# Optimization experiments

Hardware: AMD Instinct MI355X
Metric: run time of the kernel (lower is better)

## Reference

```python
import jax, jax.numpy as jnp
import numpy as np

EPS_BN = 1e-5
EPS_NORM = 1e-12
NUM_HEADS = 8


def _bn_relu(x):
    # BatchNorm2d in training mode with fresh params (gamma=1, beta=0), then ReLU.
    m = x.mean((0, 2, 3), keepdims=True)
    v = x.var((0, 2, 3), keepdims=True)  # biased variance, as PyTorch uses for normalization
    return jax.nn.relu((x - m) * jax.lax.rsqrt(v + EPS_BN))


def _conv3(x, w, groups=1):
    # 3x3 conv, stride 1, padding 1 (NCHW / OIHW)
    return jax.lax.conv_general_dilated(
        x, w, (1, 1), ((1, 1), (1, 1)),
        dimension_numbers=('NCHW', 'OIHW', 'NCHW'),
        feature_group_count=groups)


def _encoder(x, w1, w2, w3):
    # Conv1x1 -> BN -> ReLU -> Conv k2 s2 -> BN -> ReLU -> Conv1x1 -> BN -> ReLU
    x = _bn_relu(jnp.einsum('bihw,oi->bohw', x, w1))
    b, c, h, w = x.shape
    # k=2,s=2 conv as a reshape + einsum (non-overlapping 2x2 patches)
    x = _bn_relu(jnp.einsum('bchpwq,ocpq->bohw', x.reshape(b, c, h // 2, 2, w // 2, 2), w2))
    return _bn_relu(jnp.einsum('bihw,oi->bohw', x, w3))


def _decoder(x, w1, w2, w3):
    # ConvT1x1 -> BN -> ReLU -> ConvT k2 s2 -> BN -> ReLU -> ConvT1x1 -> BN -> ReLU
    x = _bn_relu(jnp.einsum('bihw,io->bohw', x, w1))
    # ConvTranspose k=2,s=2: each input pixel expands to a 2x2 block
    y = jnp.einsum('bihw,iopq->bohpwq', x, w2)
    b, o, h, p, w, q = y.shape
    x = _bn_relu(y.reshape(b, o, h * p, w * q))
    return _bn_relu(jnp.einsum('bihw,io->bohw', x, w3))


def _l2norm(x):
    # F.normalize(dim=-1) with eps=1e-12
    return x / jnp.maximum(jnp.linalg.norm(x, axis=-1, keepdims=True), EPS_NORM)


def setup_inputs() -> dict:
    key = jax.random.key(0)
    ks = jax.random.split(key, 13)
    B, C, H, W = 8, 256, 64, 64
    d = C // 4  # attention dim after self.divide

    def rn(k, shape, s=0.1):
        return jax.random.normal(k, shape, jnp.float32) * s

    return {
        'x': jax.random.normal(ks[0], (B, C, H, W), jnp.float32),
        'y': jax.random.normal(ks[1], (B, C, H, W), jnp.float32),
        'temperature': jnp.ones((NUM_HEADS, 1, 1), jnp.float32),
        'enc_w1': rn(ks[2], (d // 2, C)),
        'enc_w2': rn(ks[3], (d // 2, d // 2, 2, 2)),
        'enc_w3': rn(ks[4], (d, d // 2)),
        'kv_w': rn(ks[5], (2 * d, d)),
        'kv_dw_w': rn(ks[6], (2 * d, 1, 3, 3)),
        'q_w': rn(ks[7], (d, d)),
        'q_dw_w': rn(ks[8], (d, d, 3, 3)),
        'proj_w': rn(ks[9], (d, d)),
        'dec_w1': rn(ks[10], (d, 2 * d)),
        'dec_w2': rn(ks[11], (2 * d, 2 * d, 2, 2)),
        'dec_w3': rn(ks[12], (2 * d, 4 * d)),
    }


def reference(x, y, temperature, enc_w1, enc_w2, enc_w3, kv_w, kv_dw_w,
              q_w, q_dw_w, proj_w, dec_w1, dec_w2, dec_w3):
    # Shared freshly-built encoder applied to both x and y (same weights,
    # BN batch stats computed per call).
    x = _encoder(x, enc_w1, enc_w2, enc_w3)
    y = _encoder(y, enc_w1, enc_w2, enc_w3)
    b, c, h, w = x.shape  # c = 64, h = w = 32

    kv = _conv3(jnp.einsum('bihw,oi->bohw', x, kv_w), kv_dw_w, groups=2 * c)
    k, v = jnp.split(kv, 2, axis=1)
    q = _conv3(jnp.einsum('bihw,oi->bohw', y, q_w), q_dw_w)  # regular 3x3 conv

    ch = c // NUM_HEADS
    heads = lambda t: t.reshape(b, NUM_HEADS, ch, h * w)  # b head c (h w)
    q, k, v = heads(q), heads(k), heads(v)
    q = _l2norm(q)
    k = _l2norm(k)
    temp = temperature[None]  # [1, head, 1, 1]

    # Spatial attention: [b, head, hw, hw]
    attn_s = jax.nn.softmax(jnp.einsum('bhcn,bhcm->bhnm', q, k) * temp, axis=-1)
    out_s = jnp.einsum('bhcn,bhnm->bhcm', v, attn_s).reshape(b, c, h, w)
    out_s = jnp.einsum('bihw,oi->bohw', out_s, proj_w)

    # Channel attention: [b, head, c, c]
    attn_c = jax.nn.softmax(jnp.einsum('bhcn,bhdn->bhcd', q, k) * temp, axis=-1)
    out_c = jnp.einsum('bhcd,bhdn->bhcn', attn_c, v).reshape(b, c, h, w)
    out_c = jnp.einsum('bihw,oi->bohw', out_c, proj_w)

    return _decoder(out_s + out_c, dec_w1, dec_w2, dec_w3)
```

## Files before the change

### kernel.cpp

```cpp
#include <hip/hip_runtime.h>
#include <hip/hip_bf16.h>

#define EPS_BN 1e-5f

__global__ __launch_bounds__(256) void conv1x1_enc1_kernel(
    const float* __restrict__ in0, const float* __restrict__ in1,
    const float* __restrict__ w, float* __restrict__ out,
    float* __restrict__ stOut)
{
  __shared__ float il[32*128];
  __shared__ float wt[32*32];
  int tid  = threadIdx.x;
  int tile = blockIdx.x;
  int z    = blockIdx.y;
  int t    = z >> 3;
  const float* in  = t ? in1 : in0;
  const float* inb = in + ((size_t)(z&7))*256*4096 + tile*128;
  int cg = tid & 31;
  int og = tid >> 5;

  float acc[4][4];
#pragma unroll
  for(int j=0;j<4;j++){ acc[j][0]=acc[j][1]=acc[j][2]=acc[j][3]=0.f; }

  for(int k0=0; k0<256; k0+=32){
    __syncthreads();
#pragma unroll
    for(int u=0;u<4;u++){
      int fid = tid + u*256;
      int ch = fid >> 5, c4 = fid & 31;
      ((float4*)il)[fid] = *(const float4*)(inb + (size_t)(k0+ch)*4096 + c4*4);
    }
#pragma unroll
    for(int u=0;u<4;u++){
      int idx = tid + u*256;
      int o = idx >> 5, ch = idx & 31;
      wt[ch*32 + o] = w[(size_t)o*256 + k0 + ch];
    }
    __syncthreads();
#pragma unroll 8
    for(int ch=0; ch<32; ch++){
      float4 v  = ((float4*)il)[ch*32 + cg];
      float4 wv = ((float4*)wt)[ch*8 + og];
      acc[0][0]=fmaf(wv.x,v.x,acc[0][0]); acc[0][1]=fmaf(wv.x,v.y,acc[0][1]);
      acc[0][2]=fmaf(wv.x,v.z,acc[0][2]); acc[0][3]=fmaf(wv.x,v.w,acc[0][3]);
      acc[1][0]=fmaf(wv.y,v.x,acc[1][0]); acc[1][1]=fmaf(wv.y,v.y,acc[1][1]);
      acc[1][2]=fmaf(wv.y,v.z,acc[1][2]); acc[1][3]=fmaf(wv.y,v.w,acc[1][3]);
      acc[2][0]=fmaf(wv.z,v.x,acc[2][0]); acc[2][1]=fmaf(wv.z,v.y,acc[2][1]);
      acc[2][2]=fmaf(wv.z,v.z,acc[2][2]); acc[2][3]=fmaf(wv.z,v.w,acc[2][3]);
      acc[3][0]=fmaf(wv.w,v.x,acc[3][0]); acc[3][1]=fmaf(wv.w,v.y,acc[3][1]);
      acc[3][2]=fmaf(wv.w,v.z,acc[3][2]); acc[3][3]=fmaf(wv.w,v.w,acc[3][3]);
    }
  }

  float* ob = out + ((size_t)z*32 + og*4)*4096 + tile*128 + cg*4;
#pragma unroll
  for(int j=0;j<4;j++){
    float4 vv = {acc[j][0],acc[j][1],acc[j][2],acc[j][3]};
    *(float4*)(ob + (size_t)j*4096) = vv;
  }
#pragma unroll
  for(int j=0;j<4;j++){
    float s  = acc[j][0]+acc[j][1]+acc[j][2]+acc[j][3];
    float s2 = acc[j][0]*acc[j][0]+acc[j][1]*acc[j][1]
             + acc[j][2]*acc[j][2]+acc[j][3]*acc[j][3];
    for(int off=16; off>0; off>>=1){
      s  += __shfl_down(s,  off, 64);
      s2 += __shfl_down(s2, off, 64);
    }
    if((tid & 31)==0){
      atomicAdd(&stOut[((size_t)t*32 + og*4 + j)*2],   s);
      atomicAdd(&stOut[((size_t)t*32 + og*4 + j)*2+1], s2);
    }
  }
}

template<int OT, bool HASBN, bool HASSTATS>
__global__ __launch_bounds__(256) void conv1x1_kernel(
    const float* __restrict__ in0, const float* __restrict__ in1,
    const float* __restrict__ w, float* __restrict__ out,
    const float* __restrict__ stIn, float* __restrict__ stOut,
    int I, int O, int P, int wio, int zsplit, float invN)
{
  __shared__ float wl[2048];
  __shared__ float bnm[256], bnr[256];
  int tid = threadIdx.x;
  int o0 = blockIdx.y*OT;
  int z  = blockIdx.z;
  int t  = (z >= zsplit) ? 1 : 0;
  int b  = t ? (z - zsplit) : z;
  const float* in = t ? in1 : in0;

  for(int idx=tid; idx<I*OT; idx+=256){
    int i = idx/OT, j = idx - i*OT;
    wl[idx] = wio ? w[(size_t)i*O + o0 + j] : w[(size_t)(o0+j)*I + i];
  }
  if(HASBN){
    for(int i=tid; i<I; i+=256){
      float s  = stIn[((size_t)t*I + i)*2];
      float s2 = stIn[((size_t)t*I + i)*2+1];
      float m  = s*invN;
      bnm[i] = m;
      bnr[i] = rsqrtf(s2*invN - m*m + EPS_BN);
    }
  }
  __syncthreads();

  int p4 = blockIdx.x*256 + tid;
  const float4* inb = (const float4*)(in + (size_t)b*I*P) + p4;
  int P4 = P >> 2;

  float acc[OT][4];
#pragma unroll
  for(int j=0;j<OT;j++){ acc[j][0]=acc[j][1]=acc[j][2]=acc[j][3]=0.f; }

  float4 vb[8];
  for(int i0=0;i0<I;i0+=8){
#pragma unroll
    for(int u=0;u<8;u++) vb[u] = inb[(size_t)(i0+u)*P4];
#pragma unroll
    for(int u=0;u<8;u++){
      float4 v = vb[u];
      if(HASBN){
        float m = bnm[i0+u], r = bnr[i0+u];
        v.x = fmaxf((v.x-m)*r, 0.f); v.y = fmaxf((v.y-m)*r, 0.f);
        v.z = fmaxf((v.z-m)*r, 0.f); v.w = fmaxf((v.w-m)*r, 0.f);
      }
      const float* wr = &wl[(i0+u)*OT];
#pragma unroll
      for(int j=0;j<OT;j++){
        float wv = wr[j];
        acc[j][0] = fmaf(wv, v.x, acc[j][0]);
        acc[j][1] = fmaf(wv, v.y, acc[j][1]);
        acc[j][2] = fmaf(wv, v.z, acc[j][2]);
        acc[j][3] = fmaf(wv, v.w, acc[j][3]);
      }
    }
  }

  float4* ob = (float4*)(out + ((size_t)z*O + o0)*P) + p4;
#pragma unroll
  for(int j=0;j<OT;j++){
    float4 vv = {acc[j][0], acc[j][1], acc[j][2], acc[j][3]};
    ob[(size_t)j*P4] = vv;
  }

  if(HASSTATS){
#pragma unroll
    for(int j=0;j<OT;j++){
      float s  = acc[j][0]+acc[j][1]+acc[j][2]+acc[j][3];
      float s2 = acc[j][0]*acc[j][0]+acc[j][1]*acc[j][1]
               + acc[j][2]*acc[j][2]+acc[j][3]*acc[j][3];
      for(int off=32; off>0; off>>=1){
        s  += __shfl_down(s,  off, 64);
        s2 += __shfl_down(s2, off, 64);
      }
      if((tid & 63)==0){
        atomicAdd(&stOut[((size_t)t*O + o0 + j)*2],   s);
        atomicAdd(&stOut[((size_t)t*O + o0 + j)*2+1], s2);
      }
    }
  }
}

__global__ __launch_bounds__(256) void conv2x2s2_bn_kernel(
    const float* __restrict__ in, const float* __restrict__ w,
    float* __restrict__ out, const float* __restrict__ stIn,
    float* __restrict__ stOut, float invN)
{
  __shared__ float wl[512];
  __shared__ float bnm[32], bnr[32];
  int tid = threadIdx.x;
  int o0 = blockIdx.x*4;
  int z  = blockIdx.y;
  int t  = (z >= 8) ? 1 : 0;

  for(int idx=tid; idx<512; idx+=256){
    int pq = idx & 3, r = idx >> 2;
    int i = r >> 2, j = r & 3;
    wl[idx] = w[(((size_t)(o0+j)*32 + i)*4) + pq];
  }
  if(tid < 32){
    float s  = stIn[((size_t)t*32 + tid)*2];
    float s2 = stIn[((size_t)t*32 + tid)*2+1];
    float m  = s*invN;
    bnm[tid] = m;
    bnr[tid] = rsqrtf(s2*invN - m*m + EPS_BN);
  }
  __syncthreads();

  int h  = tid >> 3;
  int wg = tid & 7;
  int cb = wg*8;

  float acc[4][4];
#pragma unroll
  for(int j=0;j<4;j++) for(int k=0;k<4;k++) acc[j][k]=0.f;

  float4 pre[8];
  for(int i0=0;i0<32;i0+=4){
#pragma unroll
    for(int u=0;u<4;u++){
      pre[2*u]   = *(const float4*)(in + (((size_t)z*32+i0+u)*64 + 2*h)*64 + cb);
      pre[2*u+1] = *(const float4*)(in + (((size_t)z*32+i0+u)*64 + 2*h)*64 + cb + 4);
    }
#pragma unroll
    for(int u=0;u<4;u++){
      int i = i0+u;
      const float4* r1p = (const float4*)(in + (((size_t)z*32+i)*64 + 2*h+1)*64 + cb);
      float4 a0 = pre[2*u], a1 = pre[2*u+1];
      float4 b0 = r1p[0], b1 = r1p[1];
      float m = bnm[i], r = bnr[i];
      float t0[8] = {a0.x,a0.y,a0.z,a0.w,a1.x,a1.y,a1.z,a1.w};
      float t1[8] = {b0.x,b0.y,b0.z,b0.w,b1.x,b1.y,b1.z,b1.w};
#pragma unroll
      for(int e=0;e<8;e++){
        t0[e] = fmaxf((t0[e]-m)*r, 0.f);
        t1[e] = fmaxf((t1[e]-m)*r, 0.f);
      }
#pragma unroll
      for(int j=0;j<4;j++){
        const float* wj = &wl[(i*4+j)*4];
#pragma unroll
        for(int k=0;k<4;k++){
          acc[j][k] = fmaf(wj[0], t0[2*k],   acc[j][k]);
          acc[j][k] = fmaf(wj[1], t0[2*k+1], acc[j][k]);
          acc[j][k] = fmaf(wj[2], t1[2*k],   acc[j][k]);
          acc[j][k] = fmaf(wj[3], t1[2*k+1], acc[j][k]);
        }
      }
    }
  }

#pragma unroll
  for(int j=0;j<4;j++){
    float4 vv = {acc[j][0],acc[j][1],acc[j][2],acc[j][3]};
    *(float4*)(out + ((size_t)z*32 + o0+j)*1024 + h*32 + wg*4) = vv;
  }
#pragma unroll
  for(int j=0;j<4;j++){
    float s  = acc[j][0]+acc[j][1]+acc[j][2]+acc[j][3];
    float s2 = acc[j][0]*acc[j][0]+acc[j][1]*acc[j][1]
             + acc[j][2]*acc[j][2]+acc[j][3]*acc[j][3];
    for(int off=32; off>0; off>>=1){
      s  += __shfl_down(s,  off, 64);
      s2 += __shfl_down(s2, off, 64);
    }
    if((tid & 63)==0){
      atomicAdd(&stOut[((size_t)t*32 + o0 + j)*2],   s);
      atomicAdd(&stOut[((size_t)t*32 + o0 + j)*2+1], s2);
    }
  }
}

__global__ __launch_bounds__(256) void upsample2x2_bn_kernel(
    const float* __restrict__ in, const float* __restrict__ w,
    float* __restrict__ out, const float* __restrict__ stIn,
    float* __restrict__ stOut, float invN)
{
  __shared__ float wl[1024];
  __shared__ float bnm[128], bnr[128];
  int tid = threadIdx.x;
  int o0 = blockIdx.x*2;
  int b  = blockIdx.y;

  for(int idx=tid; idx<1024; idx+=256){
    int pq = idx & 3, r = idx >> 2;
    int i = r >> 1, j = r & 1;
    wl[idx] = w[((size_t)i*128 + o0+j)*4 + pq];
  }
  if(tid < 128){
    float s  = stIn[(size_t)tid*2];
    float s2 = stIn[(size_t)tid*2+1];
    float m  = s*invN;
    bnm[tid] = m;
    bnr[tid] = rsqrtf(s2*invN - m*m + EPS_BN);
  }
  __syncthreads();

  int h  = tid >> 3;
  int wg = tid & 7;
  int w0 = wg*4;

  float acc[2][16];
#pragma unroll
  for(int j=0;j<2;j++) for(int e=0;e<16;e++) acc[j][e]=0.f;

  float4 vb4[8];
  for(int i0=0;i0<128;i0+=8){
#pragma unroll
    for(int u=0;u<8;u++)
      vb4[u] = *(const float4*)(in + (((size_t)b*128+i0+u)*1024) + h*32 + w0);
#pragma unroll
    for(int u=0;u<8;u++){
      int i = i0+u;
      float4 v = vb4[u];
      float m = bnm[i], r = bnr[i];
      float vk[4] = {fmaxf((v.x-m)*r,0.f), fmaxf((v.y-m)*r,0.f),
                     fmaxf((v.z-m)*r,0.f), fmaxf((v.w-m)*r,0.f)};
#pragma unroll
      for(int j=0;j<2;j++){
        const float* wj = &wl[(i*2+j)*4];
#pragma unroll
        for(int pq=0;pq<4;pq++){
#pragma unroll
          for(int k=0;k<4;k++)
            acc[j][pq*4+k] = fmaf(wj[pq], vk[k], acc[j][pq*4+k]);
        }
      }
    }
  }

#pragma unroll
  for(int j=0;j<2;j++){
    float* ob = out + ((size_t)b*128 + o0+j)*4096;
#pragma unroll
    for(int p=0;p<2;p++){
      float4 A = {acc[j][(p*2+0)*4+0], acc[j][(p*2+1)*4+0],
                  acc[j][(p*2+0)*4+1], acc[j][(p*2+1)*4+1]};
      float4 B = {acc[j][(p*2+0)*4+2], acc[j][(p*2+1)*4+2],
                  acc[j][(p*2+0)*4+3], acc[j][(p*2+1)*4+3]};
      *(float4*)(ob + (2*h+p)*64 + 2*w0)     = A;
      *(float4*)(ob + (2*h+p)*64 + 2*w0 + 4) = B;
    }
  }

#pragma unroll
  for(int j=0;j<2;j++){
    float s=0.f, s2=0.f;
#pragma unroll
    for(int e=0;e<16;e++){ s += acc[j][e]; s2 += acc[j][e]*acc[j][e]; }
    for(int off=32; off>0; off>>=1){
      s  += __shfl_down(s,  off, 64);
      s2 += __shfl_down(s2, off, 64);
    }
    if((tid & 63)==0){
      atomicAdd(&stOut[((size_t)(o0+j))*2],   s);
      atomicAdd(&stOut[((size_t)(o0+j))*2+1], s2);
    }
  }
}

__global__ __launch_bounds__(256) void bn_final_kernel(
    float* __restrict__ x, const float* __restrict__ st, float invN)
{
  int idx4 = blockIdx.x*256 + threadIdx.x;
  int c = (idx4 >> 10) & 255;
  float s  = st[(size_t)c*2];
  float s2 = st[(size_t)c*2+1];
  float m  = s*invN;
  float r  = rsqrtf(s2*invN - m*m + EPS_BN);
  float4 v = ((float4*)x)[idx4];
  v.x = fmaxf((v.x-m)*r, 0.f); v.y = fmaxf((v.y-m)*r, 0.f);
  v.z = fmaxf((v.z-m)*r, 0.f); v.w = fmaxf((v.w-m)*r, 0.f);
  ((float4*)x)[idx4] = v;
}

__global__ __launch_bounds__(256) void dwconv3x3_kernel(
    const float* __restrict__ in, const float* __restrict__ w,
    float* __restrict__ out, int C, int H, int Wd)
{
  int idx = blockIdx.x*256 + threadIdx.x;
  int c = blockIdx.y, b = blockIdx.z;
  if(idx >= H*Wd) return;
  int h = idx / Wd, x = idx - h*Wd;
  const float* inp = in + ((size_t)b*C + c)*H*Wd;
  float acc = 0.f;
#pragma unroll
  for(int p=0;p<3;p++){
    int hh = h + p - 1;
    if((unsigned)hh >= (unsigned)H) continue;
#pragma unroll
    for(int q=0;q<3;q++){
      int wv = x + q - 1;
      if((unsigned)wv >= (unsigned)Wd) continue;
      acc += w[c*9 + p*3 + q] * inp[hh*Wd + wv];
    }
  }
  out[((size_t)b*C + c)*H*Wd + idx] = acc;
}

__global__ __launch_bounds__(256) void conv3x3_kernel(
    const float* __restrict__ in, const float* __restrict__ w,
    float* __restrict__ out, int IC, int H, int Wd)
{
  int o = blockIdx.y, b = blockIdx.z;
  __shared__ float wl[576];
  for(int t=threadIdx.x; t<IC*9; t+=256) wl[t] = w[(size_t)o*IC*9 + t];
  __syncthreads();
  int idx = blockIdx.x*256 + threadIdx.x;
  if(idx >= H*Wd) return;
  int h = idx / Wd, x = idx - h*Wd;
  const float* inb = in + (size_t)b*IC*H*Wd;
  float acc = 0.f;
  for(int i=0;i<IC;i++){
    const float* inp = inb + (size_t)i*H*Wd;
    const float* wp  = wl + i*9;
#pragma unroll
    for(int p=0;p<3;p++){
      int hh = h + p - 1;
      if((unsigned)hh >= (unsigned)H) continue;
      const float* row = inp + hh*Wd;
#pragma unroll
      for(int q=0;q<3;q++){
        int wv = x + q - 1;
        if((unsigned)wv >= (unsigned)Wd) continue;
        acc = fmaf(wp[p*3+q], row[wv], acc);
      }
    }
  }
  out[((size_t)b*gridDim.y + o)*H*Wd + idx] = acc;
}

__global__ __launch_bounds__(256) void l2norm_kernel(
    float* __restrict__ q, float* __restrict__ kv)
{
  int r = blockIdx.x;
  float* p;
  if(r < 512){ int b=r>>6, c=r&63; p = q + ((size_t)b*64+c)*1024; }
  else { int rr=r-512; int b=rr>>6, c=rr&63; p = kv + ((size_t)b*128+c)*1024; }
  int tid = threadIdx.x;
  float4 v = ((float4*)p)[tid];
  float s = v.x*v.x + v.y*v.y + v.z*v.z + v.w*v.w;
  __shared__ float ls[256];
  ls[tid]=s; __syncthreads();
  for(int st=128; st>0; st>>=1){ if(tid<st) ls[tid]+=ls[tid+st]; __syncthreads(); }
  float scale = 1.f / fmaxf(sqrtf(ls[0]), 1e-12f);
  v.x*=scale; v.y*=scale; v.z*=scale; v.w*=scale;
  ((float4*)p)[tid] = v;
}

__global__ __launch_bounds__(256) void attn_pass1(
    const float* __restrict__ q, const float* __restrict__ kv,
    const float* __restrict__ temp, float* __restrict__ den_out)
{
  int bx = blockIdx.x, hh = blockIdx.y, b = blockIdx.z;
  int nchunk = bx >> 1, mh = bx & 1;
  int tid = threadIdx.x;
  __shared__ __align__(16) float kl[512*12];
  const float* kb = kv + ((size_t)b*128 + hh*8)*1024 + mh*512;
  for(int t=tid;t<4096;t+=256){ int c=t>>9, m=t&511; kl[m*12+c]=kb[(size_t)c*1024+m]; }
  __syncthreads();
  int n = nchunk*256 + tid;
  const float* qp = q + ((size_t)b*64 + hh*8)*1024 + n;
  float th = temp[hh];
  float mxb = fabsf(th);
  float qr[8];
#pragma unroll
  for(int c=0;c<8;c++) qr[c]=qp[(size_t)c*1024]*th;
  const float4* kl4 = (const float4*)kl;
  float den = 0.f, den2 = 0.f;
  for(int m=0;m<512;m+=2){
    float4 a  = kl4[m*3],     a2 = kl4[m*3+1];
    float4 bt = kl4[(m+1)*3], b2 = kl4[(m+1)*3+1];
    float s0 = qr[0]*a.x+qr[1]*a.y+qr[2]*a.z+qr[3]*a.w
             + qr[4]*a2.x+qr[5]*a2.y+qr[6]*a2.z+qr[7]*a2.w;
    float s1 = qr[0]*bt.x+qr[1]*bt.y+qr[2]*bt.z+qr[3]*bt.w
             + qr[4]*b2.x+qr[5]*b2.y+qr[6]*b2.z+qr[7]*b2.w;
    den  += __expf(s0 - mxb);
    den2 += __expf(s1 - mxb);
  }
  atomicAdd(&den_out[((size_t)(b*8+hh))*1024+n], den+den2);
}

__global__ __launch_bounds__(256) void attn_pass2(
    const float* __restrict__ q, const float* __restrict__ kv,
    const float* __restrict__ temp, const float* __restrict__ den,
    float* __restrict__ out)
{
  int bx = blockIdx.x, hh = blockIdx.y, b = blockIdx.z;
  int mchunk = bx >> 1, nh = bx & 1;
  int tid = threadIdx.x;
  __shared__ __align__(16) float ql[512*12];
  __shared__ __align__(16) float vl[512*12];
  __shared__ float idl[512];
  int bh = b*8+hh;
  int n0 = nh*512;
  const float* qb = q  + ((size_t)b*64 + hh*8)*1024 + n0;
  const float* vb = kv + ((size_t)b*128 + 64 + hh*8)*1024 + n0;
  for(int t=tid;t<4096;t+=256){
    int c=t>>9, n=t&511;
    ql[n*12+c] = qb[(size_t)c*1024+n];
    vl[n*12+c] = vb[(size_t)c*1024+n];
  }
  for(int u=tid;u<512;u+=256) idl[u] = 1.f/den[(size_t)bh*1024 + n0 + u];
  __syncthreads();
  int m = mchunk*256 + tid;
  const float* kb = kv + ((size_t)b*128 + hh*8)*1024 + m;
  float th = temp[hh];
  float mxb = fabsf(th);
  float kr[8];
#pragma unroll
  for(int c=0;c<8;c++) kr[c]=kb[(size_t)c*1024]*th;
  float acc[8] = {0,0,0,0,0,0,0,0};
  const float4* ql4 = (const float4*)ql;
  const float4* vl4 = (const float4*)vl;
  for(int n=0;n<512;n+=2){
    float4 qa = ql4[n*3],     qa2 = ql4[n*3+1];
    float4 qb4= ql4[(n+1)*3], qb2 = ql4[(n+1)*3+1];
    float s0 = kr[0]*qa.x+kr[1]*qa.y+kr[2]*qa.z+kr[3]*qa.w
             + kr[4]*qa2.x+kr[5]*qa2.y+kr[6]*qa2.z+kr[7]*qa2.w;
    float s1 = kr[0]*qb4.x+kr[1]*qb4.y+kr[2]*qb4.z+kr[3]*qb4.w
             + kr[4]*qb2.x+kr[5]*qb2.y+kr[6]*qb2.z+kr[7]*qb2.w;
    float p0 = __expf(s0 - mxb) * idl[n];
    float p1 = __expf(s1 - mxb) * idl[n+1];
    float4 va = vl4[n*3],     va2 = vl4[n*3+1];
    float4 vb4f= vl4[(n+1)*3], vb2 = vl4[(n+1)*3+1];
    acc[0]+=p0*va.x + p1*vb4f.x; acc[1]+=p0*va.y + p1*vb4f.y;
    acc[2]+=p0*va.z + p1*vb4f.z; acc[3]+=p0*va.w + p1*vb4f.w;
    acc[4]+=p0*va2.x + p1*vb2.x; acc[5]+=p0*va2.y + p1*vb2.y;
    acc[6]+=p0*va2.z + p1*vb2.z; acc[7]+=p0*va2.w + p1*vb2.w;
  }
  float* ob = out + ((size_t)b*64 + hh*8)*1024 + m;
#pragma unroll
  for(int c=0;c<8;c++) atomicAdd(&ob[(size_t)c*1024], acc[c]);
}

__global__ __launch_bounds__(256) void attn_channel(
    const float* __restrict__ q, const float* __restrict__ kv,
    const float* __restrict__ temp, float* out)
{
  int hh = blockIdx.x, b = blockIdx.y;
  __shared__ float kl[8192];
  const float* qb = q  + ((size_t)b*64 + hh*8)*1024;
  const float* kb = kv + ((size_t)b*128 + hh*8)*1024;
  const float* vb = kv + ((size_t)b*128 + 64 + hh*8)*1024;
  int tid = threadIdx.x;
  for(int t=tid;t<8192;t+=256) kl[t]=kb[t];
  __syncthreads();
  __shared__ float part[256];
  __shared__ float a[64];
  {
    int pair = tid >> 2, seg = tid & 3;
    int c = pair >> 3, d = pair & 7;
    const float* qrow = qb + (size_t)c*1024 + seg*256;
    const float* krow = kl + d*1024 + seg*256;
    float s = 0.f;
#pragma unroll 4
    for(int n=0;n<256;n++) s += qrow[n]*krow[n];
    part[tid] = s;
  }
  __syncthreads();
  if(tid < 64){
    float g = part[tid*4]+part[tid*4+1]+part[tid*4+2]+part[tid*4+3];
    part[tid] = g * temp[hh];
  }
  __syncthreads();
  if(tid < 8){
    float mx = -3.4e38f;
    for(int d=0;d<8;d++) mx = fmaxf(mx, part[tid*8+d]);
    float den = 0.f;
    float e[8];
    for(int d=0;d<8;d++){ e[d] = __expf(part[tid*8+d]-mx); den+=e[d]; }
    float inv = 1.f/den;
    for(int d=0;d<8;d++) a[tid*8+d] = e[d]*inv;
  }
  __syncthreads();
  float* ob = out + ((size_t)b*64 + hh*8)*1024;
  for(int n=tid;n<1024;n+=256){
    float vv[8];
#pragma unroll
    for(int d=0;d<8;d++) vv[d] = vb[(size_t)d*1024+n];
#pragma unroll
    for(int c=0;c<8;c++){
      float s = 0.f;
#pragma unroll
      for(int d=0;d<8;d++) s += a[c*8+d]*vv[d];
      ob[(size_t)c*1024+n] += s;
    }
  }
}

extern "C" void kernel_launch(void* const* d_in, const int* in_sizes, int n_in,
                              void* d_out, int out_size, void* d_ws, size_t ws_size,
                              hipStream_t stream)
{
  (void)in_sizes; (void)n_in; (void)out_size; (void)ws_size;
  const float* x      = (const float*)d_in[0];
  const float* y      = (const float*)d_in[1];
  const float* temp   = (const float*)d_in[2];
  const float* enc_w1 = (const float*)d_in[3];
  const float* enc_w2 = (const float*)d_in[4];
  const float* enc_w3 = (const float*)d_in[5];
  const float* kv_w   = (const float*)d_in[6];
  const float* kv_dw_w= (const float*)d_in[7];
  const float* q_w    = (const float*)d_in[8];
  const float* q_dw_w = (const float*)d_in[9];
  const float* proj_w = (const float*)d_in[10];
  const float* dec_w1 = (const float*)d_in[11];
  const float* dec_w2 = (const float*)d_in[12];
  const float* dec_w3 = (const float*)d_in[13];
  float* out = (float*)d_out;

  float* W   = (float*)d_ws;
  float* ST  = W;
  float* ST0 = ST;
  float* ST1 = ST + 128;
  float* ST2 = ST + 256;
  float* ST3 = ST + 512;
  float* ST4 = ST + 768;
  float* ST5 = ST + 1024;
  float* A    = W + 2048;
  float* E1   = A;
  float* KV1  = A;
  float* QPre = A + 1048576;
  float* ATTN = A;
  float* PROJ = A + 524288;
  float* D1   = A + 1048576;
  float* E2   = W + 2099200;
  float* E3   = W + 2623488;
  float* KV   = W + 3672064;
  float* Q    = W + 4720640;
  float* DEN  = W + 5244928;
  float* D2   = W + 2099200;

  const float inv32k = 1.f/32768.f, inv8k = 1.f/8192.f;

  hipMemsetAsync(ST, 0, 2048*sizeof(float), stream);
  hipMemsetAsync(DEN, 0, 65536*sizeof(float), stream);

  conv1x1_enc1_kernel<<<dim3(32,16),256,0,stream>>>(x, y, enc_w1, E1, ST0);
  conv2x2s2_bn_kernel<<<dim3(8,16),256,0,stream>>>(E1, enc_w2, E2, ST0, ST1, inv32k);
  conv1x1_kernel<2,true,true><<<dim3(1,32,16),256,0,stream>>>(
      E2, E2 + (size_t)8*32*1024, enc_w3, E3, ST1, ST2, 32, 64, 1024, 0, 8, inv8k);

  conv1x1_kernel<2,true,false><<<dim3(1,64,8),256,0,stream>>>(
      E3, E3, kv_w, KV1, ST2, nullptr, 64, 128, 1024, 0, 999, inv8k);
  dwconv3x3_kernel<<<dim3(4,128,8),256,0,stream>>>(KV1, kv_dw_w, KV, 128, 32, 32);
  conv1x1_kernel<2,true,false><<<dim3(1,32,8),256,0,stream>>>(
      E3 + (size_t)8*64*1024, E3, q_w, QPre, ST2 + 128, nullptr, 64, 64, 1024, 0, 999, inv8k);
  conv3x3_kernel<<<dim3(4,64,8),256,0,stream>>>(QPre, q_dw_w, Q, 64, 32, 32);

  hipMemsetAsync(ATTN, 0, 524288*sizeof(float), stream);

  l2norm_kernel<<<1024,256,0,stream>>>(Q, KV);

  attn_pass1<<<dim3(8,8,8),256,0,stream>>>(Q, KV, temp, DEN);
  attn_pass2<<<dim3(8,8,8),256,0,stream>>>(Q, KV, temp, DEN, ATTN);
  attn_channel<<<dim3(8,8),256,0,stream>>>(Q, KV, temp, ATTN);

  conv1x1_kernel<2,false,false><<<dim3(1,32,8),256,0,stream>>>(
      ATTN, ATTN, proj_w, PROJ, nullptr, nullptr, 64, 64, 1024, 0, 999, 0.f);

  conv1x1_kernel<2,false,true><<<dim3(1,64,8),256,0,stream>>>(
      PROJ, PROJ, dec_w1, D1, nullptr, ST3, 64, 128, 1024, 1, 999, 0.f);
  upsample2x2_bn_kernel<<<dim3(64,8),256,0,stream>>>(D1, dec_w2, D2, ST3, ST4, inv8k);
  conv1x1_kernel<8,true,true><<<dim3(4,32,8),256,0,stream>>>(
      D2, D2, dec_w3, out, ST4, ST5, 128, 256, 4096, 1, 999, inv32k);
  bn_final_kernel<<<8192,256,0,stream>>>(out, ST5, inv32k);
}
```

Measured before the change: 637.5 us.

## Raise grid parallelism across encoder, small 1x1 convs and spatial attention

Result: faster. 620.8 us (-2.6%).

```diff
diff --git a/kernel.cpp b/kernel.cpp
--- a/kernel.cpp
+++ b/kernel.cpp
@@ -8,69 +8,85 @@
     const float* __restrict__ w, float* __restrict__ out,
     float* __restrict__ stOut)
 {
-  __shared__ float il[32*128];
-  __shared__ float wt[32*32];
+  __shared__ float il[2][32*64];
+  __shared__ float wt[2][32*34];
   int tid  = threadIdx.x;
   int tile = blockIdx.x;
   int z    = blockIdx.y;
   int t    = z >> 3;
   const float* in  = t ? in1 : in0;
-  const float* inb = in + ((size_t)(z&7))*256*4096 + tile*128;
-  int cg = tid & 31;
-  int og = tid >> 5;
-
-  float acc[4][4];
-#pragma unroll
-  for(int j=0;j<4;j++){ acc[j][0]=acc[j][1]=acc[j][2]=acc[j][3]=0.f; }
-
-  for(int k0=0; k0<256; k0+=32){
-    __syncthreads();
-#pragma unroll
-    for(int u=0;u<4;u++){
-      int fid = tid + u*256;
-      int ch = fid >> 5, c4 = fid & 31;
-      ((float4*)il)[fid] = *(const float4*)(inb + (size_t)(k0+ch)*4096 + c4*4);
-    }
-#pragma unroll
-    for(int u=0;u<4;u++){
-      int idx = tid + u*256;
-      int o = idx >> 5, ch = idx & 31;
-      wt[ch*32 + o] = w[(size_t)o*256 + k0 + ch];
-    }
-    __syncthreads();
+  const float* inb = in + ((size_t)(z&7))*256*4096 + tile*64;
+  int cg = tid & 15;
+  int og = tid >> 4;
+
+  float4 vr[2]; float wr[4];
+  int chA = tid >> 4;
+  int chB = 16 + chA;
+  int wo  = tid >> 5;
+  int wch = tid & 31;
+
+  vr[0] = *(const float4*)(inb + (size_t)chA*4096 + cg*4);
+  vr[1] = *(const float4*)(inb + (size_t)chB*4096 + cg*4);
+#pragma unroll
+  for(int u=0;u<4;u++) wr[u] = w[(size_t)(wo+u*8)*256 + wch];
+  ((float4*)il[0])[tid]     = vr[0];
+  ((float4*)il[0])[tid+256] = vr[1];
+#pragma unroll
+  for(int u=0;u<4;u++) wt[0][wch*34 + wo + u*8] = wr[u];
+  __syncthreads();
+
+  float acc[2][4];
+#pragma unroll
+  for(int j=0;j<2;j++){ acc[j][0]=acc[j][1]=acc[j][2]=acc[j][3]=0.f; }
+
+  for(int c=0;c<8;c++){
+    int cur = c & 1;
+    if(c < 7){
+      int k0 = (c+1)*32;
+      vr[0] = *(const float4*)(inb + (size_t)(k0+chA)*4096 + cg*4);
+      vr[1] = *(const float4*)(inb + (size_t)(k0+chB)*4096 + cg*4);
+#pragma unroll
+      for(int u=0;u<4;u++) wr[u] = w[(size_t)(wo+u*8)*256 + k0 + wch];
+    }
+    const float4* ilc = (const float4*)il[cur];
+    const float*  wtc = wt[cur];
 #pragma unroll 8
     for(int ch=0; ch<32; ch++){
-      float4 v  = ((float4*)il)[ch*32 + cg];
-      float4 wv = ((float4*)wt)[ch*8 + og];
+      float4 v  = ilc[ch*16 + cg];
+      float2 wv = *(const float2*)&wtc[ch*34 + og*2];
       acc[0][0]=fmaf(wv.x,v.x,acc[0][0]); acc[0][1]=fmaf(wv.x,v.y,acc[0][1]);
       acc[0][2]=fmaf(wv.x,v.z,acc[0][2]); acc[0][3]=fmaf(wv.x,v.w,acc[0][3]);
       acc[1][0]=fmaf(wv.y,v.x,acc[1][0]); acc[1][1]=fmaf(wv.y,v.y,acc[1][1]);
       acc[1][2]=fmaf(wv.y,v.z,acc[1][2]); acc[1][3]=fmaf(wv.y,v.w,acc[1][3]);
-      acc[2][0]=fmaf(wv.z,v.x,acc[2][0]); acc[2][1]=fmaf(wv.z,v.y,acc[2][1]);
-      acc[2][2]=fmaf(wv.z,v.z,acc[2][2]); acc[2][3]=fmaf(wv.z,v.w,acc[2][3]);
-      acc[3][0]=fmaf(wv.w,v.x,acc[3][0]); acc[3][1]=fmaf(wv.w,v.y,acc[3][1]);
-      acc[3][2]=fmaf(wv.w,v.z,acc[3][2]); acc[3][3]=fmaf(wv.w,v.w,acc[3][3]);
-    }
-  }
-
-  float* ob = out + ((size_t)z*32 + og*4)*4096 + tile*128 + cg*4;
-#pragma unroll
-  for(int j=0;j<4;j++){
+    }
+    if(c < 7){
+      int nxt = 1 - cur;
+      ((float4*)il[nxt])[tid]     = vr[0];
+      ((float4*)il[nxt])[tid+256] = vr[1];
+#pragma unroll
+      for(int u=0;u<4;u++) wt[nxt][wch*34 + wo + u*8] = wr[u];
+      __syncthreads();
+    }
+  }
+
+  float* ob = out + ((size_t)z*32 + og*2)*4096 + tile*64 + cg*4;
+#pragma unroll
+  for(int j=0;j<2;j++){
     float4 vv = {acc[j][0],acc[j][1],acc[j][2],acc[j][3]};
     *(float4*)(ob + (size_t)j*4096) = vv;
   }
 #pragma unroll
-  for(int j=0;j<4;j++){
+  for(int j=0;j<2;j++){
     float s  = acc[j][0]+acc[j][1]+acc[j][2]+acc[j][3];
     float s2 = acc[j][0]*acc[j][0]+acc[j][1]*acc[j][1]
              + acc[j][2]*acc[j][2]+acc[j][3]*acc[j][3];
-    for(int off=16; off>0; off>>=1){
-      s  += __shfl_down(s,  off, 64);
-      s2 += __shfl_down(s2, off, 64);
-    }
-    if((tid & 31)==0){
-      atomicAdd(&stOut[((size_t)t*32 + og*4 + j)*2],   s);
-      atomicAdd(&stOut[((size_t)t*32 + og*4 + j)*2+1], s2);
+    for(int off=8; off>0; off>>=1){
+      s  += __shfl_down(s,  off, 16);
+      s2 += __shfl_down(s2, off, 16);
+    }
+    if(cg==0){
+      atomicAdd(&stOut[((size_t)t*32 + og*2 + j)*2],   s);
+      atomicAdd(&stOut[((size_t)t*32 + og*2 + j)*2+1], s2);
     }
   }
 }
@@ -163,6 +179,96 @@
   }
 }
 
+template<int OT, bool HASBN, bool HASSTATS>
+__global__ __launch_bounds__(256) void conv1x1_small(
+    const float* __restrict__ in0, const float* __restrict__ in1,
+    const float* __restrict__ w, float* __restrict__ out,
+    const float* __restrict__ stIn, float* __restrict__ stOut,
+    int I, int O, int wio, int zsplit, float invN)
+{
+  __shared__ float wl[512];
+  __shared__ float bnm[128], bnr[128];
+  int tid = threadIdx.x;
+  int z  = blockIdx.z;
+  int t  = (z >= zsplit) ? 1 : 0;
+  int b  = t ? (z - zsplit) : z;
+  const float* in = t ? in1 : in0;
+  int W2 = 2*OT;
+
+  for(int idx=tid; idx<I*W2; idx+=256){
+    int i = idx/W2, slot = idx - i*W2;
+    int oabs = blockIdx.y*W2 + slot;
+    wl[idx] = wio ? w[(size_t)i*O + oabs] : w[(size_t)oabs*I + i];
+  }
+  if(HASBN){
+    for(int i=tid; i<I; i+=256){
+      float s  = stIn[((size_t)t*I + i)*2];
+      float s2 = stIn[((size_t)t*I + i)*2+1];
+      float m  = s*invN;
+      bnm[i] = m;
+      bnr[i] = rsqrtf(s2*invN - m*m + EPS_BN);
+    }
+  }
+  __syncthreads();
+
+  int p4 = blockIdx.x*128 + (tid & 127);
+  int os = tid >> 7;
+  const float4* inb = (const float4*)(in + (size_t)b*I*1024) + p4;
+
+  float acc[OT][4];
+#pragma unroll
+  for(int j=0;j<OT;j++){ acc[j][0]=acc[j][1]=acc[j][2]=acc[j][3]=0.f; }
+
+  float4 vb[8];
+  for(int i0=0;i0<I;i0+=8){
+#pragma unroll
+    for(int u=0;u<8;u++) vb[u] = inb[(size_t)(i0+u)*256];
+#pragma unroll
+    for(int u=0;u<8;u++){
+      float4 v = vb[u];
+      if(HASBN){
+        float m = bnm[i0+u], r = bnr[i0+u];
+        v.x = fmaxf((v.x-m)*r, 0.f); v.y = fmaxf((v.y-m)*r, 0.f);
+        v.z = fmaxf((v.z-m)*r, 0.f); v.w = fmaxf((v.w-m)*r, 0.f);
+      }
+      const float* wr = &wl[(i0+u)*W2 + os*OT];
+#pragma unroll
+      for(int j=0;j<OT;j++){
+        float wv = wr[j];
+        acc[j][0] = fmaf(wv, v.x, acc[j][0]);
+        acc[j][1] = fmaf(wv, v.y, acc[j][1]);
+        acc[j][2] = fmaf(wv, v.z, acc[j][2]);
+        acc[j][3] = fmaf(wv, v.w, acc[j][3]);
+      }
+    }
+  }
+
+  int obase = blockIdx.y*W2 + os*OT;
+  float4* ob = (float4*)(out + ((size_t)z*O + obase)*1024) + p4;
+#pragma unroll
+  for(int j=0;j<OT;j++){
+    float4 vv = {acc[j][0], acc[j][1], acc[j][2], acc[j][3]};
+    ob[(size_t)j*256] = vv;
+  }
+
+  if(HASSTATS){
+#pragma unroll
+    for(int j=0;j<OT;j++){
+      float s  = acc[j][0]+acc[j][1]+acc[j][2]+acc[j][3];
+      float s2 = acc[j][0]*acc[j][0]+acc[j][1]*acc[j][1]
+               + acc[j][2]*acc[j][2]+acc[j][3]*acc[j][3];
+      for(int off=32; off>0; off>>=1){
+        s  += __shfl_down(s,  off, 64);
+        s2 += __shfl_down(s2, off, 64);
+      }
+      if((tid & 63)==0){
+        atomicAdd(&stOut[((size_t)t*O + obase + j)*2],   s);
+        atomicAdd(&stOut[((size_t)t*O + obase + j)*2+1], s2);
+      }
+    }
+  }
+}
+
 __global__ __launch_bounds__(256) void conv2x2s2_bn_kernel(
     const float* __restrict__ in, const float* __restrict__ w,
     float* __restrict__ out, const float* __restrict__ stIn,
@@ -172,13 +278,13 @@
   __shared__ float bnm[32], bnr[32];
   int tid = threadIdx.x;
   int o0 = blockIdx.x*4;
-  int z  = blockIdx.y;
-  int t  = (z >= 8) ? 1 : 0;
+  int rq = blockIdx.y;
+  int z  = blockIdx.z;
+  int t  = z >> 3;
 
   for(int idx=tid; idx<512; idx+=256){
-    int pq = idx & 3, r = idx >> 2;
-    int i = r >> 2, j = r & 3;
-    wl[idx] = w[(((size_t)(o0+j)*32 + i)*4) + pq];
+    int osub = idx>>7, ch=(idx>>2)&31, pq=idx&3;
+    wl[idx] = w[(((size_t)(o0+osub)*32 + ch)*4) + pq];
   }
   if(tid < 32){
     float s  = stIn[((size_t)t*32 + tid)*2];
@@ -189,67 +295,58 @@
   }
   __syncthreads();
 
-  int h  = tid >> 3;
-  int wg = tid & 7;
-  int cb = wg*8;
-
-  float acc[4][4];
-#pragma unroll
-  for(int j=0;j<4;j++) for(int k=0;k<4;k++) acc[j][k]=0.f;
-
-  float4 pre[8];
-  for(int i0=0;i0<32;i0+=4){
-#pragma unroll
-    for(int u=0;u<4;u++){
-      pre[2*u]   = *(const float4*)(in + (((size_t)z*32+i0+u)*64 + 2*h)*64 + cb);
-      pre[2*u+1] = *(const float4*)(in + (((size_t)z*32+i0+u)*64 + 2*h)*64 + cb + 4);
-    }
-#pragma unroll
-    for(int u=0;u<4;u++){
-      int i = i0+u;
-      const float4* r1p = (const float4*)(in + (((size_t)z*32+i)*64 + 2*h+1)*64 + cb);
-      float4 a0 = pre[2*u], a1 = pre[2*u+1];
-      float4 b0 = r1p[0], b1 = r1p[1];
-      float m = bnm[i], r = bnr[i];
-      float t0[8] = {a0.x,a0.y,a0.z,a0.w,a1.x,a1.y,a1.z,a1.w};
-      float t1[8] = {b0.x,b0.y,b0.z,b0.w,b1.x,b1.y,b1.z,b1.w};
-#pragma unroll
-      for(int e=0;e<8;e++){
-        t0[e] = fmaxf((t0[e]-m)*r, 0.f);
-        t1[e] = fmaxf((t1[e]-m)*r, 0.f);
-      }
-#pragma unroll
-      for(int j=0;j<4;j++){
-        const float* wj = &wl[(i*4+j)*4];
-#pragma unroll
-        for(int k=0;k<4;k++){
-          acc[j][k] = fmaf(wj[0], t0[2*k],   acc[j][k]);
-          acc[j][k] = fmaf(wj[1], t0[2*k+1], acc[j][k]);
-          acc[j][k] = fmaf(wj[2], t1[2*k],   acc[j][k]);
-          acc[j][k] = fmaf(wj[3], t1[2*k+1], acc[j][k]);
-        }
-      }
-    }
-  }
-
-#pragma unroll
-  for(int j=0;j<4;j++){
-    float4 vv = {acc[j][0],acc[j][1],acc[j][2],acc[j][3]};
-    *(float4*)(out + ((size_t)z*32 + o0+j)*1024 + h*32 + wg*4) = vv;
-  }
-#pragma unroll
-  for(int j=0;j<4;j++){
-    float s  = acc[j][0]+acc[j][1]+acc[j][2]+acc[j][3];
-    float s2 = acc[j][0]*acc[j][0]+acc[j][1]*acc[j][1]
-             + acc[j][2]*acc[j][2]+acc[j][3]*acc[j][3];
-    for(int off=32; off>0; off>>=1){
-      s  += __shfl_down(s,  off, 64);
-      s2 += __shfl_down(s2, off, 64);
-    }
-    if((tid & 63)==0){
-      atomicAdd(&stOut[((size_t)t*32 + o0 + j)*2],   s);
-      atomicAdd(&stOut[((size_t)t*32 + o0 + j)*2+1], s2);
-    }
+  int os   = tid >> 6;
+  int slot = tid & 63;
+  int h    = rq*8 + (slot>>3);
+  int wg   = slot & 7;
+  int cb   = wg*8;
+  const float* wbase = &wl[os*128];
+  const float* inz = in + (size_t)z*32*4096;
+
+  float acc[4] = {0,0,0,0};
+  float4 c0,c1,c2,c3, n0_,n1_,n2_,n3_;
+  c0 = *(const float4*)(inz + (size_t)0*4096 + (2*h)*64 + cb);
+  c1 = *(const float4*)(inz + (size_t)0*4096 + (2*h)*64 + cb + 4);
+  c2 = *(const float4*)(inz + (size_t)0*4096 + (2*h+1)*64 + cb);
+  c3 = *(const float4*)(inz + (size_t)0*4096 + (2*h+1)*64 + cb + 4);
+  for(int ch=0; ch<32; ch++){
+    if(ch < 31){
+      n0_ = *(const float4*)(inz + (size_t)(ch+1)*4096 + (2*h)*64 + cb);
+      n1_ = *(const float4*)(inz + (size_t)(ch+1)*4096 + (2*h)*64 + cb + 4);
+      n2_ = *(const float4*)(inz + (size_t)(ch+1)*4096 + (2*h+1)*64 + cb);
+      n3_ = *(const float4*)(inz + (size_t)(ch+1)*4096 + (2*h+1)*64 + cb + 4);
+    }
+    float m = bnm[ch], r = bnr[ch];
+    float t0[8] = {c0.x,c0.y,c0.z,c0.w,c1.x,c1.y,c1.z,c1.w};
+    float t1[8] = {c2.x,c2.y,c2.z,c2.w,c3.x,c3.y,c3.z,c3.w};
+#pragma unroll
+    for(int e=0;e<8;e++){
+      t0[e] = fmaxf((t0[e]-m)*r, 0.f);
+      t1[e] = fmaxf((t1[e]-m)*r, 0.f);
+    }
+    const float* wp = wbase + ch*4;
+#pragma unroll
+    for(int k=0;k<4;k++){
+      acc[k] = fmaf(wp[0], t0[2*k],   acc[k]);
+      acc[k] = fmaf(wp[1], t0[2*k+1], acc[k]);
+      acc[k] = fmaf(wp[2], t1[2*k],   acc[k]);
+      acc[k] = fmaf(wp[3], t1[2*k+1], acc[k]);
+    }
+    c0=n0_; c1=n1_; c2=n2_; c3=n3_;
+  }
+
+  float4 vv = {acc[0],acc[1],acc[2],acc[3]};
+  *(float4*)(out + ((size_t)z*32 + o0+os)*1024 + h*32 + wg*4) = vv;
+
+  float s  = acc[0]+acc[1]+acc[2]+acc[3];
+  float s2 = acc[0]*acc[0]+acc[1]*acc[1]+acc[2]*acc[2]+acc[3]*acc[3];
+  for(int off=32; off>0; off>>=1){
+    s  += __shfl_down(s,  off, 64);
+    s2 += __shfl_down(s2, off, 64);
+  }
+  if((tid & 63)==0){
+    atomicAdd(&stOut[((size_t)t*32 + o0 + os)*2],   s);
+    atomicAdd(&stOut[((size_t)t*32 + o0 + os)*2+1], s2);
   }
 }
 
@@ -435,11 +532,11 @@
     const float* __restrict__ temp, float* __restrict__ den_out)
 {
   int bx = blockIdx.x, hh = blockIdx.y, b = blockIdx.z;
-  int nchunk = bx >> 1, mh = bx & 1;
+  int nchunk = bx >> 2, mq = bx & 3;
   int tid = threadIdx.x;
-  __shared__ __align__(16) float kl[512*12];
-  const float* kb = kv + ((size_t)b*128 + hh*8)*1024 + mh*512;
-  for(int t=tid;t<4096;t+=256){ int c=t>>9, m=t&511; kl[m*12+c]=kb[(size_t)c*1024+m]; }
+  __shared__ __align__(16) float kl[256*12];
+  const float* kb = kv + ((size_t)b*128 + hh*8)*1024 + mq*256;
+  for(int t=tid;t<2048;t+=256){ int c=t>>8, m=t&255; kl[m*12+c]=kb[(size_t)c*1024+m]; }
   __syncthreads();
   int n = nchunk*256 + tid;
   const float* qp = q + ((size_t)b*64 + hh*8)*1024 + n;
@@ -450,7 +547,7 @@
   for(int c=0;c<8;c++) qr[c]=qp[(size_t)c*1024]*th;
   const float4* kl4 = (const float4*)kl;
   float den = 0.f, den2 = 0.f;
-  for(int m=0;m<512;m+=2){
+  for(int m=0;m<256;m+=2){
     float4 a  = kl4[m*3],     a2 = kl4[m*3+1];
     float4 bt = kl4[(m+1)*3], b2 = kl4[(m+1)*3+1];
     float s0 = qr[0]*a.x+qr[1]*a.y+qr[2]*a.z+qr[3]*a.w
@@ -469,21 +566,21 @@
     float* __restrict__ out)
 {
   int bx = blockIdx.x, hh = blockIdx.y, b = blockIdx.z;
-  int mchunk = bx >> 1, nh = bx & 1;
+  int mchunk = bx >> 2, nq = bx & 3;
   int tid = threadIdx.x;
-  __shared__ __align__(16) float ql[512*12];
-  __shared__ __align__(16) float vl[512*12];
-  __shared__ float idl[512];
+  __shared__ __align__(16) float ql[256*12];
+  __shared__ __align__(16) float vl[256*12];
+  __shared__ float idl[256];
   int bh = b*8+hh;
-  int n0 = nh*512;
+  int n0 = nq*256;
   const float* qb = q  + ((size_t)b*64 + hh*8)*1024 + n0;
   const float* vb = kv + ((size_t)b*128 + 64 + hh*8)*1024 + n0;
-  for(int t=tid;t<4096;t+=256){
-    int c=t>>9, n=t&511;
+  for(int t=tid;t<2048;t+=256){
+    int c=t>>8, n=t&255;
     ql[n*12+c] = qb[(size_t)c*1024+n];
     vl[n*12+c] = vb[(size_t)c*1024+n];
   }
-  for(int u=tid;u<512;u+=256) idl[u] = 1.f/den[(size_t)bh*1024 + n0 + u];
+  idl[tid] = 1.f/den[(size_t)bh*1024 + n0 + tid];
   __syncthreads();
   int m = mchunk*256 + tid;
   const float* kb = kv + ((size_t)b*128 + hh*8)*1024 + m;
@@ -495,21 +592,21 @@
   float acc[8] = {0,0,0,0,0,0,0,0};
   const float4* ql4 = (const float4*)ql;
   const float4* vl4 = (const float4*)vl;
-  for(int n=0;n<512;n+=2){
+  for(int n=0;n<256;n+=2){
     float4 qa = ql4[n*3],     qa2 = ql4[n*3+1];
-    float4 qb4= ql4[(n+1)*3], qb2 = ql4[(n+1)*3+1];
+    float4 qc = ql4[(n+1)*3], qc2 = ql4[(n+1)*3+1];
     float s0 = kr[0]*qa.x+kr[1]*qa.y+kr[2]*qa.z+kr[3]*qa.w
              + kr[4]*qa2.x+kr[5]*qa2.y+kr[6]*qa2.z+kr[7]*qa2.w;
-    float s1 = kr[0]*qb4.x+kr[1]*qb4.y+kr[2]*qb4.z+kr[3]*qb4.w
-             + kr[4]*qb2.x+kr[5]*qb2.y+kr[6]*qb2.z+kr[7]*qb2.w;
+    float s1 = kr[0]*qc.x+kr[1]*qc.y+kr[2]*qc.z+kr[3]*qc.w
+             + kr[4]*qc2.x+kr[5]*qc2.y+kr[6]*qc2.z+kr[7]*qc2.w;
     float p0 = __expf(s0 - mxb) * idl[n];
     float p1 = __expf(s1 - mxb) * idl[n+1];
     float4 va = vl4[n*3],     va2 = vl4[n*3+1];
-    float4 vb4f= vl4[(n+1)*3], vb2 = vl4[(n+1)*3+1];
-    acc[0]+=p0*va.x + p1*vb4f.x; acc[1]+=p0*va.y + p1*vb4f.y;
-    acc[2]+=p0*va.z + p1*vb4f.z; acc[3]+=p0*va.w + p1*vb4f.w;
-    acc[4]+=p0*va2.x + p1*vb2.x; acc[5]+=p0*va2.y + p1*vb2.y;
-    acc[6]+=p0*va2.z + p1*vb2.z; acc[7]+=p0*va2.w + p1*vb2.w;
+    float4 vc = vl4[(n+1)*3], vc2 = vl4[(n+1)*3+1];
+    acc[0]+=p0*va.x + p1*vc.x; acc[1]+=p0*va.y + p1*vc.y;
+    acc[2]+=p0*va.z + p1*vc.z; acc[3]+=p0*va.w + p1*vc.w;
+    acc[4]+=p0*va2.x + p1*vc2.x; acc[5]+=p0*va2.y + p1*vc2.y;
+    acc[6]+=p0*va2.z + p1*vc2.z; acc[7]+=p0*va2.w + p1*vc2.w;
   }
   float* ob = out + ((size_t)b*64 + hh*8)*1024 + m;
 #pragma unroll
@@ -619,31 +716,31 @@
   hipMemsetAsync(ST, 0, 2048*sizeof(float), stream);
   hipMemsetAsync(DEN, 0, 65536*sizeof(float), stream);
 
-  conv1x1_enc1_kernel<<<dim3(32,16),256,0,stream>>>(x, y, enc_w1, E1, ST0);
-  conv2x2s2_bn_kernel<<<dim3(8,16),256,0,stream>>>(E1, enc_w2, E2, ST0, ST1, inv32k);
-  conv1x1_kernel<2,true,true><<<dim3(1,32,16),256,0,stream>>>(
-      E2, E2 + (size_t)8*32*1024, enc_w3, E3, ST1, ST2, 32, 64, 1024, 0, 8, inv8k);
-
-  conv1x1_kernel<2,true,false><<<dim3(1,64,8),256,0,stream>>>(
-      E3, E3, kv_w, KV1, ST2, nullptr, 64, 128, 1024, 0, 999, inv8k);
+  conv1x1_enc1_kernel<<<dim3(64,16),256,0,stream>>>(x, y, enc_w1, E1, ST0);
+  conv2x2s2_bn_kernel<<<dim3(8,4,16),256,0,stream>>>(E1, enc_w2, E2, ST0, ST1, inv32k);
+  conv1x1_small<1,true,true><<<dim3(2,32,16),256,0,stream>>>(
+      E2, E2 + (size_t)8*32*1024, enc_w3, E3, ST1, ST2, 32, 64, 0, 8, inv8k);
+
+  conv1x1_small<1,true,false><<<dim3(2,64,8),256,0,stream>>>(
+      E3, E3, kv_w, KV1, ST2, nullptr, 64, 128, 0, 999, inv8k);
   dwconv3x3_kernel<<<dim3(4,128,8),256,0,stream>>>(KV1, kv_dw_w, KV, 128, 32, 32);
-  conv1x1_kernel<2,true,false><<<dim3(1,32,8),256,0,stream>>>(
-      E3 + (size_t)8*64*1024, E3, q_w, QPre, ST2 + 128, nullptr, 64, 64, 1024, 0, 999, inv8k);
+  conv1x1_small<1,true,false><<<dim3(2,32,8),256,0,stream>>>(
+      E3 + (size_t)8*64*1024, E3, q_w, QPre, ST2 + 128, nullptr, 64, 64, 0, 999, inv8k);
   conv3x3_kernel<<<dim3(4,64,8),256,0,stream>>>(QPre, q_dw_w, Q, 64, 32, 32);
 
   hipMemsetAsync(ATTN, 0, 524288*sizeof(float), stream);
 
   l2norm_kernel<<<1024,256,0,stream>>>(Q, KV);
 
-  attn_pass1<<<dim3(8,8,8),256,0,stream>>>(Q, KV, temp, DEN);
-  attn_pass2<<<dim3(8,8,8),256,0,stream>>>(Q, KV, temp, DEN, ATTN);
+  attn_pass1<<<dim3(16,8,8),256,0,stream>>>(Q, KV, temp, DEN);
+  attn_pass2<<<dim3(16,8,8),256,0,stream>>>(Q, KV, temp, DEN, ATTN);
   attn_channel<<<dim3(8,8),256,0,stream>>>(Q, KV, temp, ATTN);
 
-  conv1x1_kernel<2,false,false><<<dim3(1,32,8),256,0,stream>>>(
-      ATTN, ATTN, proj_w, PROJ, nullptr, nullptr, 64, 64, 1024, 0, 999, 0.f);
-
-  conv1x1_kernel<2,false,true><<<dim3(1,64,8),256,0,stream>>>(
-      PROJ, PROJ, dec_w1, D1, nullptr, ST3, 64, 128, 1024, 1, 999, 0.f);
+  conv1x1_small<1,false,false><<<dim3(2,32,8),256,0,stream>>>(
+      ATTN, ATTN, proj_w, PROJ, nullptr, nullptr, 64, 64, 0, 999, 0.f);
+
+  conv1x1_small<1,false,true><<<dim3(2,64,8),256,0,stream>>>(
+      PROJ, PROJ, dec_w1, D1, nullptr, ST3, 64, 128, 1, 999, 0.f);
   upsample2x2_bn_kernel<<<dim3(64,8),256,0,stream>>>(D1, dec_w2, D2, ST3, ST4, inv8k);
   conv1x1_kernel<8,true,true><<<dim3(4,32,8),256,0,stream>>>(
       D2, D2, dec_w3, out, ST4, ST5, 128, 256, 4096, 1, 999, inv32k);
```
